# Optimization experiments

Hardware: AMD Instinct MI355X
Metric: run time of the kernel (lower is better)

The kernel has to match this reference:

```python
import jax, jax.numpy as jnp
import numpy as np

N_NODES = 50000
N_EDGES = 800000
IN_DIM = 128
HID = 64
HEADS = 4
OUT_DIM = 128
NEG_SLOPE = 0.2


def setup_inputs() -> dict:
    key = jax.random.key(0)
    ks = jax.random.split(key, 11)
    x = jax.random.normal(ks[0], (N_NODES, IN_DIM), dtype=jnp.float32)
    edge_index = jax.random.randint(ks[1], (2, N_EDGES), 0, N_NODES, dtype=jnp.int64)
    s1 = 1.0 / np.sqrt(IN_DIM)
    s2 = 1.0 / np.sqrt(HEADS * HID)
    W1 = jax.random.normal(ks[2], (IN_DIM, HEADS * HID), dtype=jnp.float32) * s1
    a_src1 = jax.random.normal(ks[3], (HEADS, HID), dtype=jnp.float32) * s2
    a_dst1 = jax.random.normal(ks[4], (HEADS, HID), dtype=jnp.float32) * s2
    b1 = jnp.zeros((HEADS * HID,), dtype=jnp.float32)
    W2 = jax.random.normal(ks[5], (HEADS * HID, OUT_DIM), dtype=jnp.float32) * s2
    a_src2 = jax.random.normal(ks[6], (1, OUT_DIM), dtype=jnp.float32) * 0.1
    a_dst2 = jax.random.normal(ks[7], (1, OUT_DIM), dtype=jnp.float32) * 0.1
    b2 = jnp.zeros((OUT_DIM,), dtype=jnp.float32)
    return {"x": x, "edge_index": edge_index, "W1": W1, "a_src1": a_src1,
            "a_dst1": a_dst1, "b1": b1, "W2": W2, "a_src2": a_src2,
            "a_dst2": a_dst2, "b2": b2}


def _gat_conv(x, src, dst, W, a_src, a_dst, bias, heads, out_per_head, concat):
    n = x.shape[0]
    # linear projection per head: [N, H, F]
    h = (x @ W).reshape(n, heads, out_per_head)
    # per-node attention terms: [N, H]
    alpha_src = jnp.einsum('nhf,hf->nh', h, a_src)
    alpha_dst = jnp.einsum('nhf,hf->nh', h, a_dst)
    # edge logits with LeakyReLU: [E, H]
    e = jax.nn.leaky_relu(alpha_src[src] + alpha_dst[dst], NEG_SLOPE)
    # softmax over incoming edges of each destination node
    m = jax.ops.segment_max(e, dst, num_segments=n)  # [N, H]
    m = jnp.where(jnp.isfinite(m), m, 0.0)
    e = jnp.exp(e - m[dst])
    denom = jax.ops.segment_sum(e, dst, num_segments=n)  # [N, H]
    alpha = e / (denom[dst] + 1e-16)  # [E, H]
    # weighted scatter-aggregate of source messages
    out = jax.ops.segment_sum(h[src] * alpha[:, :, None], dst, num_segments=n)  # [N, H, F]
    if concat:
        out = out.reshape(n, heads * out_per_head)
    else:
        out = out.mean(axis=1)
    return out + bias


def reference(x, edge_index, W1, a_src1, a_dst1, b1, W2, a_src2, a_dst2, b2):
    n = x.shape[0]
    # PyG GATConv adds self-loops by default
    loops = jnp.arange(n, dtype=edge_index.dtype)
    src = jnp.concatenate([edge_index[0], loops])
    dst = jnp.concatenate([edge_index[1], loops])
    # dropout layers are identity in inference
    h = _gat_conv(x, src, dst, W1, a_src1, a_dst1, b1, HEADS, HID, True)
    h = jax.nn.elu(h)
    out = _gat_conv(h, src, dst, W2, a_src2, a_dst2, b2, 1, OUT_DIM, True)
    # F.normalize(p=2, dim=1)
    norm = jnp.linalg.norm(out, axis=1, keepdims=True)
    return out / jnp.maximum(norm, 1e-12)
```

## Files before the change

### kernel.cpp

```cpp
#include <hip/hip_runtime.h>
#include <hip/hip_fp16.h>
#include <math.h>

#define N_NODES 50000
#define N_EDGES 800000
#define ET (N_EDGES + N_NODES)
#define IN_DIM 128
#define HID 64
#define HEADS 4
#define C1 (HEADS * HID)
#define OUT_DIM 128
#define NEG_SLOPE 0.2f
#define MTILES 3125
#define SCAN_B 1024
#define NSCB 49

typedef _Float16 h8 __attribute__((ext_vector_type(8)));
typedef float f4 __attribute__((ext_vector_type(4)));

__device__ __forceinline__ float leaky(float v) { return fmaxf(v, NEG_SLOPE * v); }
__device__ __forceinline__ float elu(float v) { return v > 0.0f ? v : expm1f(v); }

__device__ __forceinline__ void fma_mix8(float* acc, h8 v, float w) {
    union { h8 h; int i[4]; } u; u.h = v;
#pragma unroll
    for (int k = 0; k < 4; ++k) {
        asm("v_fma_mix_f32 %0, %1, %2, %0 op_sel:[0,0,0] op_sel_hi:[1,0,0]"
            : "+v"(acc[2 * k]) : "v"(u.i[k]), "v"(w));
        asm("v_fma_mix_f32 %0, %1, %2, %0 op_sel:[1,0,0] op_sel_hi:[1,0,0]"
            : "+v"(acc[2 * k + 1]) : "v"(u.i[k]), "v"(w));
    }
}

__global__ void prep_kernel(const float* __restrict__ W1, const float* __restrict__ W2,
                            const int* __restrict__ dst, __half* __restrict__ w1t,
                            __half* __restrict__ w2t, int* __restrict__ cnt) {
    const int tid = blockIdx.x * blockDim.x + threadIdx.x;
    const int np = gridDim.x * blockDim.x;
    for (int i = tid; i < IN_DIM * C1; i += np) {
        int k1 = i >> 8, n1 = i & 255;
        w1t[n1 * IN_DIM + k1] = __float2half(W1[i]);
        int k2 = i >> 7, n2 = i & 127;
        w2t[n2 * C1 + k2] = __float2half(W2[i]);
    }
    for (int i = tid; i < ET; i += np) {
        int d = (i < N_EDGES) ? dst[i] : i - N_EDGES;
        atomicAdd(&cnt[d], 1);
    }
}

__global__ void scan_local(const int* __restrict__ cnt, int* __restrict__ lscan,
                           int* __restrict__ bsum) {
    __shared__ int wsum[16];
    const int t = threadIdx.x, lane = t & 63, wv = t >> 6;
    int idx = blockIdx.x * SCAN_B + t;
    int v = (idx < N_NODES) ? cnt[idx] : 0;
    int sc = v;
#pragma unroll
    for (int o = 1; o < 64; o <<= 1) {
        int u = __shfl_up(sc, o);
        if (lane >= o) sc += u;
    }
    if (lane == 63) wsum[wv] = sc;
    __syncthreads();
    if (t == 0) {
        int run = 0;
#pragma unroll
        for (int w = 0; w < 16; ++w) { int s = wsum[w]; wsum[w] = run; run += s; }
        bsum[blockIdx.x] = run;
    }
    __syncthreads();
    if (idx < N_NODES) lscan[idx] = sc + wsum[wv];
}

__global__ void scan_bsum(int* __restrict__ bsum) {
    const int t = threadIdx.x;
    int v = (t < NSCB) ? bsum[t] : 0;
    int sc = v;
#pragma unroll
    for (int o = 1; o < 64; o <<= 1) {
        int u = __shfl_up(sc, o);
        if (t >= o) sc += u;
    }
    if (t < NSCB) bsum[t] = sc - v;
}

__global__ void scan_final(const int* __restrict__ cnt, const int* __restrict__ lscan,
                           const int* __restrict__ bsum, int* __restrict__ rp,
                           int* __restrict__ cursor) {
    int idx = blockIdx.x * SCAN_B + threadIdx.x;
    if (idx == 0) rp[0] = 0;
    if (idx >= N_NODES) return;
    int inc = lscan[idx] + bsum[idx >> 10];
    rp[idx + 1] = inc;
    cursor[idx] = inc - cnt[idx];
}

__global__ void scatter_kernel(const int* __restrict__ src, const int* __restrict__ dst,
                               int* __restrict__ cursor, int* __restrict__ col_src) {
    int i = blockIdx.x * blockDim.x + threadIdx.x;
    if (i >= ET) return;
    int s, d;
    if (i < N_EDGES) { s = src[i]; d = dst[i]; } else { s = d = i - N_EDGES; }
    int pos = atomicAdd(&cursor[d], 1);
    col_src[pos] = s;
}

__global__ __launch_bounds__(256) void gemm1_mfma(
        const float* __restrict__ x, const __half* __restrict__ w1t,
        const float* __restrict__ aws, const float* __restrict__ awd,
        __half* __restrict__ hm, float* __restrict__ as1m, float* __restrict__ ad1m) {
    const int tile = blockIdx.x * 4 + (threadIdx.x >> 6);
    if (tile >= MTILES) return;
    const int lane = threadIdx.x & 63;
    const int m0 = tile * 16, lm = lane & 15, lq = lane >> 4;
    h8 afrag[4];
    const float4* xrow = (const float4*)(x + (size_t)(m0 + lm) * IN_DIM + lq * 8);
#pragma unroll
    for (int kt = 0; kt < 4; ++kt) {
        float4 a = xrow[kt * 8];
        float4 b = xrow[kt * 8 + 1];
        union { h8 v; __half2 p[4]; } u;
        u.p[0] = __floats2half2_rn(a.x, a.y);
        u.p[1] = __floats2half2_rn(a.z, a.w);
        u.p[2] = __floats2half2_rn(b.x, b.y);
        u.p[3] = __floats2half2_rn(b.z, b.w);
        afrag[kt] = u.v;
    }
    f4 acc[16];
#pragma unroll
    for (int nt = 0; nt < 16; ++nt) acc[nt] = (f4){0.f, 0.f, 0.f, 0.f};
#pragma unroll
    for (int nt = 0; nt < 16; ++nt) {
        const h8* brow = (const h8*)(w1t + (size_t)(nt * 16 + lm) * IN_DIM + lq * 8);
#pragma unroll
        for (int kt = 0; kt < 4; ++kt)
            acc[nt] = __builtin_amdgcn_mfma_f32_16x16x32_f16(afrag[kt], brow[kt * 4],
                                                             acc[nt], 0, 0, 0);
    }
    float sS[4][4] = {{0.f}}, sD[4][4] = {{0.f}};
#pragma unroll
    for (int nt = 0; nt < 16; ++nt) {
        int col = nt * 16 + lm;
        float wa = aws[col], wd = awd[col];
        int hd = nt >> 2;
        int f = col & 63;
#pragma unroll
        for (int r = 0; r < 4; ++r) {
            float v = acc[nt][r];
            hm[((size_t)hd * N_NODES + (m0 + lq * 4 + r)) * 64 + f] = __float2half(v);
            sS[hd][r] += v * wa;
            sD[hd][r] += v * wd;
        }
    }
#pragma unroll
    for (int o = 1; o < 16; o <<= 1) {
#pragma unroll
        for (int hd = 0; hd < 4; ++hd)
#pragma unroll
            for (int r = 0; r < 4; ++r) {
                sS[hd][r] += __shfl_xor(sS[hd][r], o);
                sD[hd][r] += __shfl_xor(sD[hd][r], o);
            }
    }
    if (lm == 0) {
#pragma unroll
        for (int r = 0; r < 4; ++r) {
            int row = m0 + lq * 4 + r;
#pragma unroll
            for (int hd = 0; hd < 4; ++hd) {
                as1m[hd * N_NODES + row] = sS[hd][r];
                ad1m[hd * N_NODES + row] = sD[hd][r];
            }
        }
    }
}

__global__ __launch_bounds__(256) void gemm2_mfma(
        const __half* __restrict__ ah, const __half* __restrict__ w2t,
        const float* __restrict__ aws, const float* __restrict__ awd,
        __half* __restrict__ h, float* __restrict__ as2, float* __restrict__ ad2) {
    const int tile = blockIdx.x * 4 + (threadIdx.x >> 6);
    if (tile >= MTILES) return;
    const int lane = threadIdx.x & 63;
    const int m0 = tile * 16, lm = lane & 15, lq = lane >> 4;
    h8 afrag[8];
    const h8* arow = (const h8*)(ah + (size_t)(m0 + lm) * C1 + lq * 8);
#pragma unroll
    for (int kt = 0; kt < 8; ++kt) afrag[kt] = arow[kt * 4];
    f4 acc[8];
#pragma unroll
    for (int nt = 0; nt < 8; ++nt) acc[nt] = (f4){0.f, 0.f, 0.f, 0.f};
#pragma unroll
    for (int nt = 0; nt < 8; ++nt) {
        const h8* brow = (const h8*)(w2t + (size_t)(nt * 16 + lm) * C1 + lq * 8);
#pragma unroll
        for (int kt = 0; kt < 8; ++kt)
            acc[nt] = __builtin_amdgcn_mfma_f32_16x16x32_f16(afrag[kt], brow[kt * 4],
                                                             acc[nt], 0, 0, 0);
    }
    float sS[4] = {0.f, 0.f, 0.f, 0.f}, sD[4] = {0.f, 0.f, 0.f, 0.f};
#pragma unroll
    for (int nt = 0; nt < 8; ++nt) {
        int col = nt * 16 + lm;
        float wa = aws[col], wd = awd[col];
#pragma unroll
        for (int r = 0; r < 4; ++r) {
            float v = acc[nt][r];
            h[(size_t)(m0 + lq * 4 + r) * OUT_DIM + col] = __float2half(v);
            sS[r] += v * wa;
            sD[r] += v * wd;
        }
    }
#pragma unroll
    for (int o = 1; o < 16; o <<= 1) {
#pragma unroll
        for (int r = 0; r < 4; ++r) {
            sS[r] += __shfl_xor(sS[r], o);
            sD[r] += __shfl_xor(sD[r], o);
        }
    }
    if (lm == 0) {
#pragma unroll
        for (int r = 0; r < 4; ++r) {
            int row = m0 + lq * 4 + r;
            as2[row] = sS[r];
            ad2[row] = sD[r];
        }
    }
}

__global__ __launch_bounds__(256) void aggregate1_fused(
        const int* __restrict__ rp, const int* __restrict__ cs,
        const __half* __restrict__ h1hm, const float* __restrict__ as1m,
        const float* __restrict__ ad1m, const float* __restrict__ b1,
        __half* __restrict__ out1h) {
    __shared__ int2 stg[8][32];
    const int head = blockIdx.x & 3, g = blockIdx.x >> 2;
    const int hw = threadIdx.x >> 5, li = threadIdx.x & 31;
    const int d = g * 8 + hw;
    const int e0 = rp[d], deg = rp[d + 1] - e0;
    const float* asb = as1m + head * N_NODES;
    const float adv = ad1m[head * N_NODES + d];
    const char* hb = (const char*)h1hm + (size_t)head * N_NODES * 128;
    const int es = li >> 3, fl = li & 7;
    const int lbyte = fl * 16;
    float acc[8] = {0.f, 0.f, 0.f, 0.f, 0.f, 0.f, 0.f, 0.f};
    float dsum = 0.f;
    for (int c0 = 0; c0 < deg; c0 += 32) {
        const int clen = min(32, deg - c0);
        int idx = c0 + li;
        bool valid = idx < deg;
        int s = valid ? cs[e0 + idx] : 0;
        float x = valid ? __expf(leaky(asb[s] + adv)) : 0.f;
        stg[hw][li] = make_int2(s << 7, __float_as_int(x));
        dsum += x;
        __builtin_amdgcn_wave_barrier();
        int j = 0;
        for (; j + 8 <= clen; j += 8) {
            int2 p0 = stg[hw][j + es];
            int2 p1 = stg[hw][j + 4 + es];
            h8 v0 = *(const h8*)(hb + p0.x + lbyte);
            h8 v1 = *(const h8*)(hb + p1.x + lbyte);
            fma_mix8(acc, v0, __int_as_float(p0.y));
            fma_mix8(acc, v1, __int_as_float(p1.y));
        }
        for (; j < clen; j += 4) {
            int2 p0 = stg[hw][j + es];
            h8 v0 = *(const h8*)(hb + p0.x + lbyte);
            fma_mix8(acc, v0, __int_as_float(p0.y));
        }
        __builtin_amdgcn_wave_barrier();
    }
#pragma unroll
    for (int f = 0; f < 8; ++f) {
        acc[f] += __shfl_xor(acc[f], 8);
        acc[f] += __shfl_xor(acc[f], 16);
    }
#pragma unroll
    for (int o = 16; o > 0; o >>= 1) dsum += __shfl_xor(dsum, o);
    if (es == 0) {
        float inv = 1.0f / (dsum + 1e-16f);
        float4 bA = ((const float4*)b1)[head * 16 + fl * 2];
        float4 bB = ((const float4*)b1)[head * 16 + fl * 2 + 1];
        h8 o;
        o[0] = (_Float16)elu(acc[0] * inv + bA.x);
        o[1] = (_Float16)elu(acc[1] * inv + bA.y);
        o[2] = (_Float16)elu(acc[2] * inv + bA.z);
        o[3] = (_Float16)elu(acc[3] * inv + bA.w);
        o[4] = (_Float16)elu(acc[4] * inv + bB.x);
        o[5] = (_Float16)elu(acc[5] * inv + bB.y);
        o[6] = (_Float16)elu(acc[6] * inv + bB.z);
        o[7] = (_Float16)elu(acc[7] * inv + bB.w);
        *(h8*)((char*)out1h + (size_t)d * 512 + head * 128 + lbyte) = o;
    }
}

__global__ __launch_bounds__(256) void aggregate2_fused(
        const int* __restrict__ rp, const int* __restrict__ cs,
        const __half* __restrict__ h2h, const float* __restrict__ as2,
        const float* __restrict__ ad2, const float* __restrict__ b2,
        float* __restrict__ out) {
    __shared__ int2 stg[8][32];
    const int hw = threadIdx.x >> 5, li = threadIdx.x & 31;
    const int d = blockIdx.x * 8 + hw;
    const int e0 = rp[d], deg = rp[d + 1] - e0;
    const float adv = ad2[d];
    const int q = li >> 4, lo = li & 15;
    const int lbyte = lo * 16;
    const char* hbase = (const char*)h2h;
    float acc[8] = {0.f, 0.f, 0.f, 0.f, 0.f, 0.f, 0.f, 0.f};
    float dsum = 0.f;
    for (int c0 = 0; c0 < deg; c0 += 32) {
        const int clen = min(32, deg - c0);
        int idx = c0 + li;
        bool valid = idx < deg;
        int s = valid ? cs[e0 + idx] : 0;
        float x = valid ? __expf(leaky(as2[s] + adv)) : 0.f;
        stg[hw][li] = make_int2(valid ? (s << 8) : 0, __float_as_int(x));
        dsum += x;
        __builtin_amdgcn_wave_barrier();
        int j = 0;
        for (; j + 4 <= clen; j += 4) {
            int2 p0 = stg[hw][j + q];
            int2 p1 = stg[hw][j + 2 + q];
            h8 v0 = *(const h8*)(hbase + p0.x + lbyte);
            h8 v1 = *(const h8*)(hbase + p1.x + lbyte);
            fma_mix8(acc, v0, __int_as_float(p0.y));
            fma_mix8(acc, v1, __int_as_float(p1.y));
        }
        for (; j < clen; j += 2) {
            int2 p0 = stg[hw][j + q];
            h8 v0 = *(const h8*)(hbase + p0.x + lbyte);
            fma_mix8(acc, v0, __int_as_float(p0.y));
        }
        __builtin_amdgcn_wave_barrier();
    }
#pragma unroll
    for (int f = 0; f < 8; ++f) acc[f] += __shfl_xor(acc[f], 16);
#pragma unroll
    for (int o = 16; o > 0; o >>= 1) dsum += __shfl_xor(dsum, o);
    if (q == 0) {
        float inv = 1.0f / (dsum + 1e-16f);
        float4 bA = ((const float4*)b2)[lo * 2];
        float4 bB = ((const float4*)b2)[lo * 2 + 1];
        float v0 = acc[0] * inv + bA.x, v1 = acc[1] * inv + bA.y;
        float v2 = acc[2] * inv + bA.z, v3 = acc[3] * inv + bA.w;
        float v4 = acc[4] * inv + bB.x, v5 = acc[5] * inv + bB.y;
        float v6 = acc[6] * inv + bB.z, v7 = acc[7] * inv + bB.w;
        float ss = v0 * v0 + v1 * v1 + v2 * v2 + v3 * v3 +
                   v4 * v4 + v5 * v5 + v6 * v6 + v7 * v7;
#pragma unroll
        for (int o = 1; o < 16; o <<= 1) ss += __shfl_xor(ss, o);
        float sc = 1.0f / fmaxf(sqrtf(ss), 1e-12f);
        float4* orow = (float4*)((char*)out + (size_t)d * 512 + lo * 32);
        orow[0] = make_float4(v0 * sc, v1 * sc, v2 * sc, v3 * sc);
        orow[1] = make_float4(v4 * sc, v5 * sc, v6 * sc, v7 * sc);
    }
}

extern "C" void kernel_launch(void* const* d_in, const int* in_sizes, int n_in,
                              void* d_out, int out_size, void* d_ws, size_t ws_size,
                              hipStream_t stream) {
    const float* x     = (const float*)d_in[0];
    const int*   edge  = (const int*)d_in[1];
    const int*   src   = edge;
    const int*   dst   = edge + N_EDGES;
    const float* W1    = (const float*)d_in[2];
    const float* aw_s1 = (const float*)d_in[3];
    const float* aw_d1 = (const float*)d_in[4];
    const float* b1    = (const float*)d_in[5];
    const float* W2    = (const float*)d_in[6];
    const float* aw_s2 = (const float*)d_in[7];
    const float* aw_d2 = (const float*)d_in[8];
    const float* b2    = (const float*)d_in[9];
    float* out = (float*)d_out;

    char* ws = (char*)d_ws;
    size_t off = 0;
    auto alloc = [&](size_t bytes) {
        void* p = ws + off;
        off += (bytes + 255) & ~(size_t)255;
        return p;
    };
    int*    col_src = (int*)alloc((size_t)ET * 4);
    int*    rp     = (int*)alloc((size_t)(N_NODES + 1) * 4);
    int*    cursor = (int*)alloc((size_t)N_NODES * 4);
    int*    cnt    = (int*)alloc((size_t)N_NODES * 4);
    int*    lscan  = (int*)alloc((size_t)NSCB * SCAN_B * 4);
    int*    bsum   = (int*)alloc((size_t)NSCB * 4);
    float*  as1    = (float*)alloc((size_t)N_NODES * HEADS * 4);
    float*  ad1    = (float*)alloc((size_t)N_NODES * HEADS * 4);
    float*  as2    = (float*)alloc((size_t)N_NODES * 4);
    float*  ad2    = (float*)alloc((size_t)N_NODES * 4);
    __half* w1t    = (__half*)alloc((size_t)IN_DIM * C1 * 2);
    __half* w2t    = (__half*)alloc((size_t)C1 * OUT_DIM * 2);
    __half* h1hm   = (__half*)alloc((size_t)N_NODES * C1 * 2);
    __half* out1h  = (__half*)alloc((size_t)N_NODES * C1 * 2);
    __half* h2h    = h1hm;
    (void)off;

    hipMemsetAsync(cnt, 0, (size_t)N_NODES * 4, stream);

    const int egrid = (ET + 255) / 256;

    prep_kernel<<<1024, 256, 0, stream>>>(W1, W2, dst, w1t, w2t, cnt);
    scan_local<<<NSCB, SCAN_B, 0, stream>>>(cnt, lscan, bsum);
    scan_bsum<<<1, 64, 0, stream>>>(bsum);
    scan_final<<<NSCB, SCAN_B, 0, stream>>>(cnt, lscan, bsum, rp, cursor);
    scatter_kernel<<<egrid, 256, 0, stream>>>(src, dst, cursor, col_src);

    gemm1_mfma<<<(MTILES + 3) / 4, 256, 0, stream>>>(x, w1t, aw_s1, aw_d1, h1hm, as1, ad1);
    aggregate1_fused<<<(N_NODES / 8) * HEADS, 256, 0, stream>>>(rp, col_src, h1hm, as1, ad1, b1, out1h);

    gemm2_mfma<<<(MTILES + 3) / 4, 256, 0, stream>>>(out1h, w2t, aw_s2, aw_d2, h2h, as2, ad2);
    aggregate2_fused<<<N_NODES / 8, 256, 0, stream>>>(rp, col_src, h2h, as2, ad2, b2, out);
}
```

Before: 356.4 us.

## Store 16-bit source indices, swap MFMA operands, precompute layer-1 edge weights, unroll gathers

The CSR source-index array is now stored as 16-bit values. Node ids below 65536 fit in that width, which halves the index traffic read by both aggregation passes. Both GEMMs swap the MFMA operands so each lane holds four consecutive output columns of one node. That allows vectorised half-precision stores and a cheaper two-step shuffle reduction for the attention dot products. A new alpha1 kernel computes the exponentiated layer-1 edge logits once for all four heads, so the four per-head aggregation blocks no longer each do the random as1 gather and the exp. This costs an extra pass and a 4×ET float buffer written and read back. The gather loops in both aggregation kernels are also unrolled further to keep more loads in flight.

```diff
diff --git a/kernel.cpp b/kernel.cpp
--- a/kernel.cpp
+++ b/kernel.cpp
@@ -17,6 +17,7 @@
 
 typedef _Float16 h8 __attribute__((ext_vector_type(8)));
 typedef float f4 __attribute__((ext_vector_type(4)));
+typedef unsigned short u16;
 
 __device__ __forceinline__ float leaky(float v) { return fmaxf(v, NEG_SLOPE * v); }
 __device__ __forceinline__ float elu(float v) { return v > 0.0f ? v : expm1f(v); }
@@ -97,13 +98,13 @@
 }
 
 __global__ void scatter_kernel(const int* __restrict__ src, const int* __restrict__ dst,
-                               int* __restrict__ cursor, int* __restrict__ col_src) {
+                               int* __restrict__ cursor, u16* __restrict__ cs16) {
     int i = blockIdx.x * blockDim.x + threadIdx.x;
     if (i >= ET) return;
     int s, d;
     if (i < N_EDGES) { s = src[i]; d = dst[i]; } else { s = d = i - N_EDGES; }
     int pos = atomicAdd(&cursor[d], 1);
-    col_src[pos] = s;
+    cs16[pos] = (u16)s;
 }
 
 __global__ __launch_bounds__(256) void gemm1_mfma(
@@ -114,8 +115,9 @@
     if (tile >= MTILES) return;
     const int lane = threadIdx.x & 63;
     const int m0 = tile * 16, lm = lane & 15, lq = lane >> 4;
+    const int node = m0 + lm;
     h8 afrag[4];
-    const float4* xrow = (const float4*)(x + (size_t)(m0 + lm) * IN_DIM + lq * 8);
+    const float4* xrow = (const float4*)(x + (size_t)node * IN_DIM + lq * 8);
 #pragma unroll
     for (int kt = 0; kt < 4; ++kt) {
         float4 a = xrow[kt * 8];
@@ -135,43 +137,35 @@
         const h8* brow = (const h8*)(w1t + (size_t)(nt * 16 + lm) * IN_DIM + lq * 8);
 #pragma unroll
         for (int kt = 0; kt < 4; ++kt)
-            acc[nt] = __builtin_amdgcn_mfma_f32_16x16x32_f16(afrag[kt], brow[kt * 4],
+            acc[nt] = __builtin_amdgcn_mfma_f32_16x16x32_f16(brow[kt * 4], afrag[kt],
                                                              acc[nt], 0, 0, 0);
     }
-    float sS[4][4] = {{0.f}}, sD[4][4] = {{0.f}};
+    float sS[4] = {0.f, 0.f, 0.f, 0.f}, sD[4] = {0.f, 0.f, 0.f, 0.f};
 #pragma unroll
     for (int nt = 0; nt < 16; ++nt) {
-        int col = nt * 16 + lm;
-        float wa = aws[col], wd = awd[col];
-        int hd = nt >> 2;
-        int f = col & 63;
-#pragma unroll
-        for (int r = 0; r < 4; ++r) {
-            float v = acc[nt][r];
-            hm[((size_t)hd * N_NODES + (m0 + lq * 4 + r)) * 64 + f] = __float2half(v);
-            sS[hd][r] += v * wa;
-            sD[hd][r] += v * wd;
-        }
-    }
-#pragma unroll
-    for (int o = 1; o < 16; o <<= 1) {
-#pragma unroll
-        for (int hd = 0; hd < 4; ++hd)
-#pragma unroll
-            for (int r = 0; r < 4; ++r) {
-                sS[hd][r] += __shfl_xor(sS[hd][r], o);
-                sD[hd][r] += __shfl_xor(sD[hd][r], o);
-            }
-    }
-    if (lm == 0) {
-#pragma unroll
-        for (int r = 0; r < 4; ++r) {
-            int row = m0 + lq * 4 + r;
-#pragma unroll
-            for (int hd = 0; hd < 4; ++hd) {
-                as1m[hd * N_NODES + row] = sS[hd][r];
-                ad1m[hd * N_NODES + row] = sD[hd][r];
-            }
+        const int col0 = nt * 16 + lq * 4;
+        float4 wa4 = ((const float4*)aws)[nt * 4 + lq];
+        float4 wd4 = ((const float4*)awd)[nt * 4 + lq];
+        union { __half2 h2[2]; int2 i2; } u;
+        u.h2[0] = __floats2half2_rn(acc[nt][0], acc[nt][1]);
+        u.h2[1] = __floats2half2_rn(acc[nt][2], acc[nt][3]);
+        const int head = col0 >> 6;
+        *(int2*)((char*)hm + ((size_t)head * N_NODES + node) * 128 + (col0 & 63) * 2) = u.i2;
+        sS[nt >> 2] += acc[nt][0] * wa4.x + acc[nt][1] * wa4.y +
+                       acc[nt][2] * wa4.z + acc[nt][3] * wa4.w;
+        sD[nt >> 2] += acc[nt][0] * wd4.x + acc[nt][1] * wd4.y +
+                       acc[nt][2] * wd4.z + acc[nt][3] * wd4.w;
+    }
+#pragma unroll
+    for (int h = 0; h < 4; ++h) {
+        sS[h] += __shfl_xor(sS[h], 16); sS[h] += __shfl_xor(sS[h], 32);
+        sD[h] += __shfl_xor(sD[h], 16); sD[h] += __shfl_xor(sD[h], 32);
+    }
+    if (lq == 0) {
+#pragma unroll
+        for (int h = 0; h < 4; ++h) {
+            as1m[h * N_NODES + node] = sS[h];
+            ad1m[h * N_NODES + node] = sD[h];
         }
     }
 }
@@ -184,8 +178,9 @@
     if (tile >= MTILES) return;
     const int lane = threadIdx.x & 63;
     const int m0 = tile * 16, lm = lane & 15, lq = lane >> 4;
+    const int node = m0 + lm;
     h8 afrag[8];
-    const h8* arow = (const h8*)(ah + (size_t)(m0 + lm) * C1 + lq * 8);
+    const h8* arow = (const h8*)(ah + (size_t)node * C1 + lq * 8);
 #pragma unroll
     for (int kt = 0; kt < 8; ++kt) afrag[kt] = arow[kt * 4];
     f4 acc[8];
@@ -196,53 +191,64 @@
         const h8* brow = (const h8*)(w2t + (size_t)(nt * 16 + lm) * C1 + lq * 8);
 #pragma unroll
         for (int kt = 0; kt < 8; ++kt)
-            acc[nt] = __builtin_amdgcn_mfma_f32_16x16x32_f16(afrag[kt], brow[kt * 4],
+            acc[nt] = __builtin_amdgcn_mfma_f32_16x16x32_f16(brow[kt * 4], afrag[kt],
                                                              acc[nt], 0, 0, 0);
     }
-    float sS[4] = {0.f, 0.f, 0.f, 0.f}, sD[4] = {0.f, 0.f, 0.f, 0.f};
+    float sS = 0.f, sD = 0.f;
 #pragma unroll
     for (int nt = 0; nt < 8; ++nt) {
-        int col = nt * 16 + lm;
-        float wa = aws[col], wd = awd[col];
-#pragma unroll
-        for (int r = 0; r < 4; ++r) {
-            float v = acc[nt][r];
-            h[(size_t)(m0 + lq * 4 + r) * OUT_DIM + col] = __float2half(v);
-            sS[r] += v * wa;
-            sD[r] += v * wd;
-        }
-    }
-#pragma unroll
-    for (int o = 1; o < 16; o <<= 1) {
-#pragma unroll
-        for (int r = 0; r < 4; ++r) {
-            sS[r] += __shfl_xor(sS[r], o);
-            sD[r] += __shfl_xor(sD[r], o);
-        }
-    }
-    if (lm == 0) {
-#pragma unroll
-        for (int r = 0; r < 4; ++r) {
-            int row = m0 + lq * 4 + r;
-            as2[row] = sS[r];
-            ad2[row] = sD[r];
-        }
+        const int col0 = nt * 16 + lq * 4;
+        float4 wa4 = ((const float4*)aws)[nt * 4 + lq];
+        float4 wd4 = ((const float4*)awd)[nt * 4 + lq];
+        union { __half2 h2[2]; int2 i2; } u;
+        u.h2[0] = __floats2half2_rn(acc[nt][0], acc[nt][1]);
+        u.h2[1] = __floats2half2_rn(acc[nt][2], acc[nt][3]);
+        *(int2*)((char*)h + (size_t)node * (OUT_DIM * 2) + col0 * 2) = u.i2;
+        sS += acc[nt][0] * wa4.x + acc[nt][1] * wa4.y +
+              acc[nt][2] * wa4.z + acc[nt][3] * wa4.w;
+        sD += acc[nt][0] * wd4.x + acc[nt][1] * wd4.y +
+              acc[nt][2] * wd4.z + acc[nt][3] * wd4.w;
+    }
+    sS += __shfl_xor(sS, 16); sS += __shfl_xor(sS, 32);
+    sD += __shfl_xor(sD, 16); sD += __shfl_xor(sD, 32);
+    if (lq == 0) {
+        as2[node] = sS;
+        ad2[node] = sD;
+    }
+}
+
+__global__ __launch_bounds__(256) void alpha1_kernel(
+        const int* __restrict__ rp, const u16* __restrict__ cs16,
+        const float* __restrict__ as1m, const float* __restrict__ ad1m,
+        float* __restrict__ alphaP) {
+    const int hw = threadIdx.x >> 5, li = threadIdx.x & 31;
+    const int d = blockIdx.x * 8 + hw;
+    const int e0 = rp[d], deg = rp[d + 1] - e0;
+    const float a0 = ad1m[d];
+    const float a1 = ad1m[N_NODES + d];
+    const float a2 = ad1m[2 * N_NODES + d];
+    const float a3 = ad1m[3 * N_NODES + d];
+    for (int idx = li; idx < deg; idx += 32) {
+        int p = e0 + idx;
+        int s = cs16[p];
+        alphaP[p]            = __expf(leaky(as1m[s] + a0));
+        alphaP[ET + p]       = __expf(leaky(as1m[N_NODES + s] + a1));
+        alphaP[2 * ET + p]   = __expf(leaky(as1m[2 * N_NODES + s] + a2));
+        alphaP[3 * ET + p]   = __expf(leaky(as1m[3 * N_NODES + s] + a3));
     }
 }
 
 __global__ __launch_bounds__(256) void aggregate1_fused(
-        const int* __restrict__ rp, const int* __restrict__ cs,
-        const __half* __restrict__ h1hm, const float* __restrict__ as1m,
-        const float* __restrict__ ad1m, const float* __restrict__ b1,
-        __half* __restrict__ out1h) {
+        const int* __restrict__ rp, const u16* __restrict__ cs16,
+        const float* __restrict__ alphaP, const __half* __restrict__ hm,
+        const float* __restrict__ b1, __half* __restrict__ out1h) {
     __shared__ int2 stg[8][32];
     const int head = blockIdx.x & 3, g = blockIdx.x >> 2;
     const int hw = threadIdx.x >> 5, li = threadIdx.x & 31;
     const int d = g * 8 + hw;
     const int e0 = rp[d], deg = rp[d + 1] - e0;
-    const float* asb = as1m + head * N_NODES;
-    const float adv = ad1m[head * N_NODES + d];
-    const char* hb = (const char*)h1hm + (size_t)head * N_NODES * 128;
+    const float* ap = alphaP + (size_t)head * ET;
+    const char* hb = (const char*)hm + (size_t)head * N_NODES * 128;
     const int es = li >> 3, fl = li & 7;
     const int lbyte = fl * 16;
     float acc[8] = {0.f, 0.f, 0.f, 0.f, 0.f, 0.f, 0.f, 0.f};
@@ -251,19 +257,25 @@
         const int clen = min(32, deg - c0);
         int idx = c0 + li;
         bool valid = idx < deg;
-        int s = valid ? cs[e0 + idx] : 0;
-        float x = valid ? __expf(leaky(asb[s] + adv)) : 0.f;
-        stg[hw][li] = make_int2(s << 7, __float_as_int(x));
-        dsum += x;
+        int s = valid ? (int)cs16[e0 + idx] : 0;
+        float a = valid ? ap[e0 + idx] : 0.f;
+        stg[hw][li] = make_int2(s << 7, __float_as_int(a));
+        dsum += a;
         __builtin_amdgcn_wave_barrier();
         int j = 0;
-        for (; j + 8 <= clen; j += 8) {
+        for (; j + 16 <= clen; j += 16) {
             int2 p0 = stg[hw][j + es];
             int2 p1 = stg[hw][j + 4 + es];
+            int2 p2 = stg[hw][j + 8 + es];
+            int2 p3 = stg[hw][j + 12 + es];
             h8 v0 = *(const h8*)(hb + p0.x + lbyte);
             h8 v1 = *(const h8*)(hb + p1.x + lbyte);
+            h8 v2 = *(const h8*)(hb + p2.x + lbyte);
+            h8 v3 = *(const h8*)(hb + p3.x + lbyte);
             fma_mix8(acc, v0, __int_as_float(p0.y));
             fma_mix8(acc, v1, __int_as_float(p1.y));
+            fma_mix8(acc, v2, __int_as_float(p2.y));
+            fma_mix8(acc, v3, __int_as_float(p3.y));
         }
         for (; j < clen; j += 4) {
             int2 p0 = stg[hw][j + es];
@@ -297,7 +309,7 @@
 }
 
 __global__ __launch_bounds__(256) void aggregate2_fused(
-        const int* __restrict__ rp, const int* __restrict__ cs,
+        const int* __restrict__ rp, const u16* __restrict__ cs16,
         const __half* __restrict__ h2h, const float* __restrict__ as2,
         const float* __restrict__ ad2, const float* __restrict__ b2,
         float* __restrict__ out) {
@@ -315,19 +327,25 @@
         const int clen = min(32, deg - c0);
         int idx = c0 + li;
         bool valid = idx < deg;
-        int s = valid ? cs[e0 + idx] : 0;
-        float x = valid ? __expf(leaky(as2[s] + adv)) : 0.f;
-        stg[hw][li] = make_int2(valid ? (s << 8) : 0, __float_as_int(x));
-        dsum += x;
+        int s = valid ? (int)cs16[e0 + idx] : 0;
+        float xv = valid ? __expf(leaky(as2[s] + adv)) : 0.f;
+        stg[hw][li] = make_int2(s << 8, __float_as_int(xv));
+        dsum += xv;
         __builtin_amdgcn_wave_barrier();
         int j = 0;
-        for (; j + 4 <= clen; j += 4) {
+        for (; j + 8 <= clen; j += 8) {
             int2 p0 = stg[hw][j + q];
             int2 p1 = stg[hw][j + 2 + q];
+            int2 p2 = stg[hw][j + 4 + q];
+            int2 p3 = stg[hw][j + 6 + q];
             h8 v0 = *(const h8*)(hbase + p0.x + lbyte);
             h8 v1 = *(const h8*)(hbase + p1.x + lbyte);
+            h8 v2 = *(const h8*)(hbase + p2.x + lbyte);
+            h8 v3 = *(const h8*)(hbase + p3.x + lbyte);
             fma_mix8(acc, v0, __int_as_float(p0.y));
             fma_mix8(acc, v1, __int_as_float(p1.y));
+            fma_mix8(acc, v2, __int_as_float(p2.y));
+            fma_mix8(acc, v3, __int_as_float(p3.y));
         }
         for (; j < clen; j += 2) {
             int2 p0 = stg[hw][j + q];
@@ -383,21 +401,22 @@
         off += (bytes + 255) & ~(size_t)255;
         return p;
     };
-    int*    col_src = (int*)alloc((size_t)ET * 4);
+    u16*    cs16   = (u16*)alloc((size_t)ET * 2);
     int*    rp     = (int*)alloc((size_t)(N_NODES + 1) * 4);
     int*    cursor = (int*)alloc((size_t)N_NODES * 4);
     int*    cnt    = (int*)alloc((size_t)N_NODES * 4);
     int*    lscan  = (int*)alloc((size_t)NSCB * SCAN_B * 4);
     int*    bsum   = (int*)alloc((size_t)NSCB * 4);
-    float*  as1    = (float*)alloc((size_t)N_NODES * HEADS * 4);
-    float*  ad1    = (float*)alloc((size_t)N_NODES * HEADS * 4);
+    float*  as1m   = (float*)alloc((size_t)N_NODES * HEADS * 4);
+    float*  ad1m   = (float*)alloc((size_t)N_NODES * HEADS * 4);
     float*  as2    = (float*)alloc((size_t)N_NODES * 4);
     float*  ad2    = (float*)alloc((size_t)N_NODES * 4);
     __half* w1t    = (__half*)alloc((size_t)IN_DIM * C1 * 2);
     __half* w2t    = (__half*)alloc((size_t)C1 * OUT_DIM * 2);
-    __half* h1hm   = (__half*)alloc((size_t)N_NODES * C1 * 2);
+    float*  alphaP = (float*)alloc((size_t)HEADS * ET * 4);
+    __half* hm     = (__half*)alloc((size_t)N_NODES * C1 * 2);
     __half* out1h  = (__half*)alloc((size_t)N_NODES * C1 * 2);
-    __half* h2h    = h1hm;
+    __half* h2h    = hm;
     (void)off;
 
     hipMemsetAsync(cnt, 0, (size_t)N_NODES * 4, stream);
@@ -408,11 +427,12 @@
     scan_local<<<NSCB, SCAN_B, 0, stream>>>(cnt, lscan, bsum);
     scan_bsum<<<1, 64, 0, stream>>>(bsum);
     scan_final<<<NSCB, SCAN_B, 0, stream>>>(cnt, lscan, bsum, rp, cursor);
-    scatter_kernel<<<egrid, 256, 0, stream>>>(src, dst, cursor, col_src);
-
-    gemm1_mfma<<<(MTILES + 3) / 4, 256, 0, stream>>>(x, w1t, aw_s1, aw_d1, h1hm, as1, ad1);
-    aggregate1_fused<<<(N_NODES / 8) * HEADS, 256, 0, stream>>>(rp, col_src, h1hm, as1, ad1, b1, out1h);
+    scatter_kernel<<<egrid, 256, 0, stream>>>(src, dst, cursor, cs16);
+
+    gemm1_mfma<<<(MTILES + 3) / 4, 256, 0, stream>>>(x, w1t, aw_s1, aw_d1, hm, as1m, ad1m);
+    alpha1_kernel<<<N_NODES / 8, 256, 0, stream>>>(rp, cs16, as1m, ad1m, alphaP);
+    aggregate1_fused<<<(N_NODES / 8) * HEADS, 256, 0, stream>>>(rp, cs16, alphaP, hm, b1, out1h);
 
     gemm2_mfma<<<(MTILES + 3) / 4, 256, 0, stream>>>(out1h, w2t, aw_s2, aw_d2, h2h, as2, ad2);
-    aggregate2_fused<<<N_NODES / 8, 256, 0, stream>>>(rp, col_src, h2h, as2, ad2, b2, out);
-}
+    aggregate2_fused<<<N_NODES / 8, 256, 0, stream>>>(rp, cs16, h2h, as2, ad2, b2, out);
+}
```

Measured after the change: 389.7 us. +9.3%, slower.
